# Optimization experiments

Hardware: AMD Instinct MI355X
Metric: run time of the kernel (lower is better)

Reference implementation:

```python
import jax, jax.numpy as jnp
import numpy as np
import math

NUM_V = 32; NUM_K = 16; DK = 128; DV = 128; KCONV = 4; H = 2048
KEY_DIM = NUM_K * DK          # 2048
VALUE_DIM = NUM_V * DV        # 4096
CONV_DIM = 2 * KEY_DIM + VALUE_DIM  # 8192
EPS = 1e-6
VPK = NUM_V // NUM_K


def setup_inputs() -> dict:
    key = jax.random.key(0)
    ks = jax.random.split(key, 12)
    s = 0.02  # weight scale for numerical sanity
    return {
        "hidden_in": jax.random.normal(ks[0], (1, 1, H), jnp.float32),
        "conv_state": jax.random.normal(ks[1], (1, CONV_DIM, KCONV), jnp.float32),
        "rec_state": jax.random.normal(ks[2], (1, NUM_V, DK, DV), jnp.float32) * s,
        "W_qkv": jax.random.normal(ks[3], (CONV_DIM, H), jnp.float32) * s,
        "W_z": jax.random.normal(ks[4], (VALUE_DIM, H), jnp.float32) * s,
        "W_b": jax.random.normal(ks[5], (NUM_V, H), jnp.float32) * s,
        "W_a": jax.random.normal(ks[6], (NUM_V, H), jnp.float32) * s,
        "W_out": jax.random.normal(ks[7], (H, VALUE_DIM), jnp.float32) * s,
        "conv_w": jax.random.normal(ks[8], (CONV_DIM, KCONV), jnp.float32) * s,
        "dt_bias": jax.random.normal(ks[9], (NUM_V,), jnp.float32),
        "A_log": jax.random.normal(ks[10], (NUM_V,), jnp.float32),
        "norm_w": jnp.ones((DV,), jnp.float32),
    }


def _l2norm(x, eps=1e-6):
    return x * jax.lax.rsqrt(jnp.sum(x * x, axis=-1, keepdims=True) + eps)


def reference(hidden_in, conv_state, rec_state, W_qkv, W_z, W_b, W_a,
              W_out, conv_w, dt_bias, A_log, norm_w):
    h = hidden_in[0, 0]                       # (H,)
    mixed = W_qkv @ h                         # (CONV_DIM,)
    z = W_z @ h                               # (VALUE_DIM,)
    b = W_b @ h                               # (NUM_V,)
    a = W_a @ h                               # (NUM_V,)

    # causal conv1d update: shift state by one, take dot with kernel
    w = jnp.concatenate([conv_state, mixed[None, :, None]], axis=-1)  # (1, C, K+1)
    new_conv_state = w[:, :, 1:]                                      # (1, C, K)
    conv_out = jax.nn.silu(jnp.sum(new_conv_state * conv_w[None], axis=-1))[0]  # (C,)

    q = conv_out[:KEY_DIM].reshape(NUM_K, DK)
    k = conv_out[KEY_DIM:2 * KEY_DIM].reshape(NUM_K, DK)
    v = conv_out[2 * KEY_DIM:].reshape(NUM_V, DV)
    q = jnp.repeat(q, VPK, axis=0)            # (NUM_V, DK)
    k = jnp.repeat(k, VPK, axis=0)

    q = _l2norm(q) * (1.0 / math.sqrt(DK))
    k = _l2norm(k)

    beta = jax.nn.sigmoid(b)                                  # (NUM_V,)
    g = -jnp.exp(A_log) * jax.nn.softplus(a + dt_bias)        # (NUM_V,)

    # gated delta-rule recurrent update
    rec = rec_state[0] * jnp.exp(g)[:, None, None]            # (NUM_V, DK, DV)
    kv_mem = jnp.einsum('hkd,hk->hd', rec, k)                 # (NUM_V, DV)
    delta = (v - kv_mem) * beta[:, None]
    rec = rec + k[:, :, None] * delta[:, None, :]
    core = jnp.einsum('hkd,hk->hd', rec, q)                   # (NUM_V, DV)

    # gated RMSNorm over Dv per head
    var = jnp.mean(core * core, axis=-1, keepdims=True)
    xn = core * jax.lax.rsqrt(var + EPS) * norm_w
    zf = z.reshape(NUM_V, DV)
    out = (xn * jax.nn.silu(zf)).reshape(VALUE_DIM)

    hidden_out = (W_out @ out).reshape(1, 1, H)
    return (hidden_out, new_conv_state, rec[None])
```

## Files before the change

kernel.cpp:

```cpp
#include <hip/hip_runtime.h>

#define HDIM 2048
#define NUM_V 32
#define NUM_K 16
#define DK 128
#define DV 128
#define KEY_DIM 2048
#define VALUE_DIM 4096
#define CONV_DIM 8192
#define TOTAL_ROWS 12352



__global__ __launch_bounds__(256) void k1_gemv(
    const float* __restrict__ h,
    const float* __restrict__ Wqkv,
    const float* __restrict__ Wz,
    const float* __restrict__ Wb,
    const float* __restrict__ Wa,
    const float* __restrict__ conv_state,
    const float* __restrict__ conv_w,
    float* __restrict__ ws,
    float* __restrict__ out_conv)
{
    const int row  = (blockIdx.x * 256 + threadIdx.x) >> 6;
    const int lane = threadIdx.x & 63;
    if (row >= TOTAL_ROWS) return;

    const float* wrow;
    if (row < 8192)       wrow = Wqkv + (size_t)row * HDIM;
    else if (row < 12288) wrow = Wz   + (size_t)(row - 8192) * HDIM;
    else if (row < 12320) wrow = Wb   + (size_t)(row - 12288) * HDIM;
    else                  wrow = Wa   + (size_t)(row - 12320) * HDIM;

    float acc = 0.f;
#pragma unroll
    for (int i = 0; i < 8; ++i) {
        const int idx = (i * 64 + lane) * 4;
        float4 w4 = *reinterpret_cast<const float4*>(wrow + idx);
        float4 h4 = *reinterpret_cast<const float4*>(h + idx);
        acc += w4.x * h4.x + w4.y * h4.y + w4.z * h4.z + w4.w * h4.w;
    }
#pragma unroll
    for (int off = 32; off > 0; off >>= 1)
        acc += __shfl_down(acc, off, 64);

    if (lane == 0) {
        if (row < 8192) {
            float4 cs = *reinterpret_cast<const float4*>(conv_state + row * 4);
            float4 cw = *reinterpret_cast<const float4*>(conv_w + row * 4);
            float pre = cs.y * cw.x + cs.z * cw.y + cs.w * cw.z + acc * cw.w;
            float co = pre / (1.f + expf(-pre));
            ws[row] = co;
            float4 ncs;
            ncs.x = cs.y; ncs.y = cs.z; ncs.z = cs.w; ncs.w = acc;
            *reinterpret_cast<float4*>(out_conv + row * 4) = ncs;
        } else {
            ws[row] = acc;
        }
    }
}

__device__ __forceinline__ float blksum128(float v, volatile float* s_red, int tid) {
#pragma unroll
    for (int off = 32; off > 0; off >>= 1)
        v += __shfl_down(v, off, 64);
    __syncthreads();
    if ((tid & 63) == 0) s_red[tid >> 6] = v;
    __syncthreads();
    return s_red[0] + s_red[1];
}

__global__ __launch_bounds__(128) void k2_rec(
    const float* __restrict__ ws,
    const float* __restrict__ rec_in,
    const float* __restrict__ dt_bias,
    const float* __restrict__ A_log,
    const float* __restrict__ norm_w,
    float* __restrict__ rec_out,
    float* __restrict__ out_vec)
{
    __shared__ float s_k[128];
    __shared__ float s_q[128];
    __shared__ float s_red[2];

    const int hh = blockIdx.x;
    const int d  = threadIdx.x;
    const int kh = hh >> 1;

    const float bv   = ws[12288 + hh];
    const float av   = ws[12320 + hh];
    const float beta = 1.f / (1.f + expf(-bv));
    const float x    = av + dt_bias[hh];
    const float sp   = fmaxf(x, 0.f) + log1pf(expf(-fabsf(x)));
    const float decay = expf(-expf(A_log[hh]) * sp);

    const float qr = ws[kh * 128 + d];
    const float kr = ws[KEY_DIM + kh * 128 + d];
    const float vv = ws[2 * KEY_DIM + hh * 128 + d];

    const float ssq = blksum128(qr * qr, s_red, d);
    const float ssk = blksum128(kr * kr, s_red, d);

    s_q[d] = qr * rsqrtf(ssq + 1e-6f) * 0.08838834764831845f;
    s_k[d] = kr * rsqrtf(ssk + 1e-6f);
    __syncthreads();

    const float* rrow = rec_in  + (size_t)hh * (DK * DV);
    float*       wrow = rec_out + (size_t)hh * (DK * DV);

    float kv = 0.f;
#pragma unroll 8
    for (int kk = 0; kk < DK; ++kk)
        kv += rrow[kk * DV + d] * s_k[kk];
    kv *= decay;
    const float delta = (vv - kv) * beta;

    float core = 0.f;
#pragma unroll 8
    for (int kk = 0; kk < DK; ++kk) {
        float r = rrow[kk * DV + d] * decay + s_k[kk] * delta;
        wrow[kk * DV + d] = r;
        core += r * s_q[kk];
    }

    const float ssc = blksum128(core * core, s_red, d);
    const float xn  = core * rsqrtf(ssc * (1.f / 128.f) + 1e-6f) * norm_w[d];
    const float zv  = ws[8192 + hh * 128 + d];
    out_vec[hh * 128 + d] = xn * (zv / (1.f + expf(-zv)));
}

__global__ __launch_bounds__(256) void k3_out(
    const float* __restrict__ Wout,
    const float* __restrict__ out_vec,
    float* __restrict__ hidden_out)
{
    const int row  = (blockIdx.x * 256 + threadIdx.x) >> 6;
    const int lane = threadIdx.x & 63;
    if (row >= HDIM) return;

    const float* wrow = Wout + (size_t)row * VALUE_DIM;
    float acc = 0.f;
#pragma unroll
    for (int i = 0; i < 16; ++i) {
        const int idx = (i * 64 + lane) * 4;
        float4 w4 = *reinterpret_cast<const float4*>(wrow + idx);
        float4 o4 = *reinterpret_cast<const float4*>(out_vec + idx);
        acc += w4.x * o4.x + w4.y * o4.y + w4.z * o4.z + w4.w * o4.w;
    }
#pragma unroll
    for (int off = 32; off > 0; off >>= 1)
        acc += __shfl_down(acc, off, 64);
    if (lane == 0) hidden_out[row] = acc;
}

extern "C" void kernel_launch(void* const* d_in, const int* in_sizes, int n_in,
                              void* d_out, int out_size, void* d_ws, size_t ws_size,
                              hipStream_t stream) {
    const float* hidden_in  = (const float*)d_in[0];
    const float* conv_state = (const float*)d_in[1];
    const float* rec_state  = (const float*)d_in[2];
    const float* W_qkv      = (const float*)d_in[3];
    const float* W_z        = (const float*)d_in[4];
    const float* W_b        = (const float*)d_in[5];
    const float* W_a        = (const float*)d_in[6];
    const float* W_out      = (const float*)d_in[7];
    const float* conv_w     = (const float*)d_in[8];
    const float* dt_bias    = (const float*)d_in[9];
    const float* A_log      = (const float*)d_in[10];
    const float* norm_w     = (const float*)d_in[11];

    float* out = (float*)d_out;
    float* ws  = (float*)d_ws;

    k1_gemv<<<TOTAL_ROWS / 4, 256, 0, stream>>>(hidden_in, W_qkv, W_z, W_b, W_a,
                                                conv_state, conv_w, ws, out + 2048);
    k2_rec<<<NUM_V, 128, 0, stream>>>(ws, rec_state, dt_bias, A_log, norm_w,
                                      out + 2048 + CONV_DIM * 4, ws + 12352);
    k3_out<<<HDIM / 4, 256, 0, stream>>>(W_out, ws + 12352, out);
}
```

Before: 38.65 us.

## Split recurrent-state update across 8 DK slices per head with 1024-thread blocks

The recurrent kernel now uses 1024 threads per head instead of 128. Each group of 128 threads handles a 16-row slice of the 128x128 state, and the partial kv and core dot products are reduced through shared memory. The aim is more memory-level parallelism on the per-head state read and write, which previously ran as a long serial 128-iteration loop per thread across only 32 blocks. The cost is extra barriers and shared-memory reductions.

```diff
diff --git a/kernel.cpp b/kernel.cpp
--- a/kernel.cpp
+++ b/kernel.cpp
@@ -61,17 +61,7 @@
     }
 }
 
-__device__ __forceinline__ float blksum128(float v, volatile float* s_red, int tid) {
-#pragma unroll
-    for (int off = 32; off > 0; off >>= 1)
-        v += __shfl_down(v, off, 64);
-    __syncthreads();
-    if ((tid & 63) == 0) s_red[tid >> 6] = v;
-    __syncthreads();
-    return s_red[0] + s_red[1];
-}
-
-__global__ __launch_bounds__(128) void k2_rec(
+__global__ __launch_bounds__(1024) void k2_rec(
     const float* __restrict__ ws,
     const float* __restrict__ rec_in,
     const float* __restrict__ dt_bias,
@@ -82,52 +72,92 @@
 {
     __shared__ float s_k[128];
     __shared__ float s_q[128];
-    __shared__ float s_red[2];
-
-    const int hh = blockIdx.x;
-    const int d  = threadIdx.x;
-    const int kh = hh >> 1;
-
-    const float bv   = ws[12288 + hh];
-    const float av   = ws[12320 + hh];
-    const float beta = 1.f / (1.f + expf(-bv));
-    const float x    = av + dt_bias[hh];
-    const float sp   = fmaxf(x, 0.f) + log1pf(expf(-fabsf(x)));
+    __shared__ float s_delta[128];
+    __shared__ float s_part[8][128];
+    __shared__ float s_red[4];
+
+    const int hh  = blockIdx.x;
+    const int t   = threadIdx.x;
+    const int d   = t & 127;
+    const int kkb = t >> 7;
+    const int kh  = hh >> 1;
+
+    const float bv    = ws[12288 + hh];
+    const float av    = ws[12320 + hh];
+    const float beta  = 1.f / (1.f + expf(-bv));
+    const float x     = av + dt_bias[hh];
+    const float sp    = fmaxf(x, 0.f) + log1pf(expf(-fabsf(x)));
     const float decay = expf(-expf(A_log[hh]) * sp);
 
-    const float qr = ws[kh * 128 + d];
-    const float kr = ws[KEY_DIM + kh * 128 + d];
-    const float vv = ws[2 * KEY_DIM + hh * 128 + d];
-
-    const float ssq = blksum128(qr * qr, s_red, d);
-    const float ssk = blksum128(kr * kr, s_red, d);
-
-    s_q[d] = qr * rsqrtf(ssq + 1e-6f) * 0.08838834764831845f;
-    s_k[d] = kr * rsqrtf(ssk + 1e-6f);
-    __syncthreads();
-
-    const float* rrow = rec_in  + (size_t)hh * (DK * DV);
-    float*       wrow = rec_out + (size_t)hh * (DK * DV);
-
-    float kv = 0.f;
-#pragma unroll 8
-    for (int kk = 0; kk < DK; ++kk)
-        kv += rrow[kk * DV + d] * s_k[kk];
-    kv *= decay;
-    const float delta = (vv - kv) * beta;
+    float qr = 0.f, kr = 0.f;
+    if (t < 128) {
+        qr = ws[kh * 128 + d];
+        kr = ws[KEY_DIM + kh * 128 + d];
+        float sq = qr * qr, sk = kr * kr;
+#pragma unroll
+        for (int off = 32; off > 0; off >>= 1) {
+            sq += __shfl_down(sq, off, 64);
+            sk += __shfl_down(sk, off, 64);
+        }
+        if ((t & 63) == 0) { s_red[t >> 6] = sq; s_red[2 + (t >> 6)] = sk; }
+    }
+    __syncthreads();
+    if (t < 128) {
+        const float ssq = s_red[0] + s_red[1];
+        const float ssk = s_red[2] + s_red[3];
+        s_q[d] = qr * rsqrtf(ssq + 1e-6f) * 0.08838834764831845f;
+        s_k[d] = kr * rsqrtf(ssk + 1e-6f);
+    }
+    __syncthreads();
+
+    const float* rrow = rec_in  + (size_t)hh * (DK * DV) + kkb * 16 * DV;
+    float*       wrow = rec_out + (size_t)hh * (DK * DV) + kkb * 16 * DV;
+
+    float kvp = 0.f;
+#pragma unroll
+    for (int i = 0; i < 16; ++i)
+        kvp += rrow[i * DV + d] * s_k[kkb * 16 + i];
+    s_part[kkb][d] = kvp;
+    __syncthreads();
+
+    if (t < 128) {
+        float kv = 0.f;
+#pragma unroll
+        for (int j = 0; j < 8; ++j) kv += s_part[j][d];
+        kv *= decay;
+        const float vv = ws[2 * KEY_DIM + hh * 128 + d];
+        s_delta[d] = (vv - kv) * beta;
+    }
+    __syncthreads();
+
+    const float dlt = s_delta[d];
+    float corep = 0.f;
+#pragma unroll
+    for (int i = 0; i < 16; ++i) {
+        const float r = rrow[i * DV + d] * decay + s_k[kkb * 16 + i] * dlt;
+        wrow[i * DV + d] = r;
+        corep += r * s_q[kkb * 16 + i];
+    }
+    s_part[kkb][d] = corep;
+    __syncthreads();
 
     float core = 0.f;
-#pragma unroll 8
-    for (int kk = 0; kk < DK; ++kk) {
-        float r = rrow[kk * DV + d] * decay + s_k[kk] * delta;
-        wrow[kk * DV + d] = r;
-        core += r * s_q[kk];
-    }
-
-    const float ssc = blksum128(core * core, s_red, d);
-    const float xn  = core * rsqrtf(ssc * (1.f / 128.f) + 1e-6f) * norm_w[d];
-    const float zv  = ws[8192 + hh * 128 + d];
-    out_vec[hh * 128 + d] = xn * (zv / (1.f + expf(-zv)));
+    if (t < 128) {
+#pragma unroll
+        for (int j = 0; j < 8; ++j) core += s_part[j][d];
+        float sc = core * core;
+#pragma unroll
+        for (int off = 32; off > 0; off >>= 1)
+            sc += __shfl_down(sc, off, 64);
+        if ((t & 63) == 0) s_red[t >> 6] = sc;
+    }
+    __syncthreads();
+    if (t < 128) {
+        const float ssc = s_red[0] + s_red[1];
+        const float xn  = core * rsqrtf(ssc * (1.f / 128.f) + 1e-6f) * norm_w[d];
+        const float zv  = ws[8192 + hh * 128 + d];
+        out_vec[hh * 128 + d] = xn * (zv / (1.f + expf(-zv)));
+    }
 }
 
 __global__ __launch_bounds__(256) void k3_out(
@@ -175,7 +205,7 @@
 
     k1_gemv<<<TOTAL_ROWS / 4, 256, 0, stream>>>(hidden_in, W_qkv, W_z, W_b, W_a,
                                                 conv_state, conv_w, ws, out + 2048);
-    k2_rec<<<NUM_V, 128, 0, stream>>>(ws, rec_state, dt_bias, A_log, norm_w,
-                                      out + 2048 + CONV_DIM * 4, ws + 12352);
+    k2_rec<<<NUM_V, 1024, 0, stream>>>(ws, rec_state, dt_bias, A_log, norm_w,
+                                       out + 2048 + CONV_DIM * 4, ws + 12352);
     k3_out<<<HDIM / 4, 256, 0, stream>>>(W_out, ws + 12352, out);
 }
```

Measured after the change: 32.67 us. 15.5% less time.
